# Kernel tuning notes

Hardware: AMD Instinct MI355X
Metric: run time of the kernel (lower is better)

The kernel has to match this reference:

```python
import jax, jax.numpy as jnp
import numpy as np
from jax import lax

TAU = 0.25
N_TIMESTEPS = 12
OUTPUT_TICKS = 4
INPUT_DIM = 1024
HIDDEN = 1024
OUTPUT_DIM = 1024
CLEANUP = 512
BATCH = 1024
W_SD = 0.1


def setup_inputs() -> dict:
    key = jax.random.key(0)
    ks = jax.random.split(key, 6)
    inputs = jax.random.normal(ks[0], (BATCH, N_TIMESTEPS, INPUT_DIM), dtype=jnp.float32)
    w_oh = W_SD * jax.random.normal(ks[1], (INPUT_DIM, HIDDEN), dtype=jnp.float32)
    w_hp = W_SD * jax.random.normal(ks[2], (HIDDEN, OUTPUT_DIM), dtype=jnp.float32)
    w_pp = W_SD * jax.random.normal(ks[3], (OUTPUT_DIM, OUTPUT_DIM), dtype=jnp.float32)
    w_pc = W_SD * jax.random.normal(ks[4], (OUTPUT_DIM, CLEANUP), dtype=jnp.float32)
    w_cp = W_SD * jax.random.normal(ks[5], (CLEANUP, OUTPUT_DIM), dtype=jnp.float32)
    bias_h = jnp.zeros((HIDDEN,), jnp.float32)
    bias_p = jnp.zeros((OUTPUT_DIM,), jnp.float32)
    bias_c = jnp.zeros((CLEANUP,), jnp.float32)
    return {"inputs": inputs, "w_oh": w_oh, "w_hp": w_hp, "w_pp": w_pp,
            "w_pc": w_pc, "w_cp": w_cp, "bias_h": bias_h, "bias_p": bias_p,
            "bias_c": bias_c}


def reference(inputs, w_oh, w_hp, w_pp, w_pc, w_cp, bias_h, bias_p, bias_c):
    B = inputs.shape[0]
    act = jax.nn.sigmoid
    # time-major input stream: step t consumes o_input[:, t-1, :]
    x = jnp.swapaxes(inputs, 0, 1)  # [T, B, I]

    in_h0 = jnp.zeros((B, HIDDEN), jnp.float32)
    in_p0 = jnp.zeros((B, OUTPUT_DIM), jnp.float32)
    in_c0 = jnp.zeros((B, CLEANUP), jnp.float32)
    carry0 = (in_h0, in_p0, in_c0, in_h0 + 0.5, in_p0 + 0.5, in_c0 + 0.5)

    def step(carry, o_t):
        in_h, in_p, in_c, a_h, a_p, a_c = carry
        # leaky-integrator blends; hp/pp/cp/pc all use PREVIOUS step activations
        h = TAU * (o_t @ w_oh + bias_h) + (1.0 - TAU) * in_h
        p = TAU * (a_h @ w_hp + a_p @ w_pp + a_c @ w_cp + bias_p) + (1.0 - TAU) * in_p
        c = TAU * (a_p @ w_pc + bias_c) + (1.0 - TAU) * in_c
        a_p_new = act(p)
        new_carry = (h, p, c, act(h), a_p_new, act(c))
        return new_carry, a_p_new

    _, act_p_seq = lax.scan(step, carry0, x)  # [T, B, OUTPUT_DIM]
    return act_p_seq[-OUTPUT_TICKS:]  # [OUTPUT_TICKS, B, OUTPUT_DIM]
```

## Files before the change

### kernel.cpp

```cpp
#include <hip/hip_runtime.h>
#include <cstdint>
#include <cstddef>


typedef _Float16 half8 __attribute__((ext_vector_type(8)));
typedef float floatx4 __attribute__((ext_vector_type(4)));

__device__ __forceinline__ void async_cp16(const void* g, void* l) {
  __builtin_amdgcn_global_load_lds(
      (const __attribute__((address_space(1))) void*)g,
      (__attribute__((address_space(3))) void*)l, 16, 0, 0);
}

__device__ __forceinline__ float sigmoidf_(float x) {
  return 1.f / (1.f + __expf(-x));
}

__global__ __launch_bounds__(256) void k_trans_all(
    const float* __restrict__ w_oh, const float* __restrict__ w_hp,
    _Float16* __restrict__ WohT, _Float16* __restrict__ Whp) {
  const float* src = blockIdx.z ? w_hp : w_oh;
  _Float16* dst = blockIdx.z ? Whp : WohT;
  __shared__ float tile[64][65];
  const int k0 = blockIdx.y * 64, n0 = blockIdx.x * 64;
  const int tx = threadIdx.x & 63, ty = threadIdx.x >> 6;
#pragma unroll
  for (int j = 0; j < 16; ++j) {
    int kr = j * 4 + ty;
    tile[kr][tx] = src[(size_t)(k0 + kr) * 1024 + n0 + tx];
  }
  __syncthreads();
#pragma unroll
  for (int j = 0; j < 16; ++j) {
    int nr = j * 4 + ty;
    dst[(size_t)(n0 + nr) * 1024 + k0 + tx] = (_Float16)tile[tx][nr];
  }
}

__global__ __launch_bounds__(256) void k_pack_all(
    const float* __restrict__ w_pp, const float* __restrict__ w_cp,
    const float* __restrict__ w_pc, _Float16* __restrict__ Wrf,
    _Float16* __restrict__ Wcf) {
  const int z = blockIdx.z;
  const float* src;
  _Float16* dst;
  int N, kStride, kOff;
  if (z == 0) {
    src = w_pp; dst = Wrf; N = 1024; kStride = 48; kOff = 0;
  } else if (z == 1) {
    if (blockIdx.y >= 8) return;
    src = w_cp; dst = Wrf; N = 1024; kStride = 48; kOff = 32;
  } else {
    if (blockIdx.x >= 8) return;
    src = w_pc; dst = Wcf; N = 512; kStride = 32; kOff = 0;
  }
  __shared__ float tile[64][65];
  const int k0 = blockIdx.y * 64, n0 = blockIdx.x * 64;
  const int tx = threadIdx.x & 63, ty = threadIdx.x >> 6;
#pragma unroll
  for (int jj = 0; jj < 16; ++jj) {
    int kr = jj * 4 + ty;
    tile[kr][tx] = src[(size_t)(k0 + kr) * N + n0 + tx];
  }
  __syncthreads();
  const int j = threadIdx.x >> 6, lane = threadIdx.x & 63;
  const int r16 = lane & 15, quad = lane >> 4;
#pragma unroll
  for (int c = 0; c < 2; ++c) {
    half8 v;
#pragma unroll
    for (int u = 0; u < 8; ++u)
      v[u] = (_Float16)tile[c * 32 + quad * 8 + u][j * 16 + r16];
    const int kcG = kOff + blockIdx.y * 2 + c;
    *(half8*)(dst + ((size_t)(blockIdx.x * kStride + kcG) * 4 + j) * 512 +
              lane * 8) = v;
  }
}

__global__ __launch_bounds__(256) void k_q0(
    const float* __restrict__ w_hp, const float* __restrict__ bias_p,
    _Float16* __restrict__ Q) {
  const int n = blockIdx.x * 256 + threadIdx.x;
  float s = 0.f;
  for (int k = 0; k < 1024; ++k) s += w_hp[(size_t)k * 1024 + n];
  const _Float16 q = (_Float16)(0.25f * (0.5f * s + bias_p[n]));
  for (int b = 0; b < 1024; ++b) Q[(size_t)b * 1024 + n] = q;
}

__global__ __launch_bounds__(256) void k_prep(
    const float* __restrict__ x, _Float16* __restrict__ U,
    _Float16* __restrict__ AP0, _Float16* __restrict__ AC0,
    float* __restrict__ Pst, float* __restrict__ Cst) {
  const int id = blockIdx.x * 256 + threadIdx.x;
  const int b = id >> 10, i = id & 1023;
  const float* xb = x + (size_t)b * 12 * 1024 + i;
  float g = 0.f;
#pragma unroll
  for (int t = 0; t < 11; ++t) {
    g = xb[t * 1024] + 0.75f * g;
    U[(size_t)t * 1048576 + id] = (_Float16)g;
  }
  AP0[id] = (_Float16)0.5f;
  Pst[id] = 0.f;
  if (i < 512) {
    const int cid = b * 512 + i;
    AC0[cid] = (_Float16)0.5f;
    Cst[cid] = 0.f;
  }
}

__global__ __launch_bounds__(256) void k_gemm_big(
    const _Float16* __restrict__ A, const _Float16* __restrict__ B,
    const float* __restrict__ bias, _Float16* __restrict__ dst, int mode) {
  __shared__ __align__(16) _Float16 sA[8192];
  __shared__ __align__(16) _Float16 sB[8192];
  const int lane = threadIdx.x & 63, w = threadIdx.x >> 6;
  const int mBase = blockIdx.y * 128, nBase = blockIdx.x * 128;
  const int r16 = lane & 15, quad = lane >> 4, mrow = lane >> 3;
  const int gsw = ((lane & 7) ^ (mrow & 7)) * 8;
  const floatx4 zero = {0.f, 0.f, 0.f, 0.f};
  floatx4 acc[4][4];
#pragma unroll
  for (int i = 0; i < 4; ++i)
#pragma unroll
    for (int j = 0; j < 4; ++j) acc[i][j] = zero;

  const _Float16* gbase =
      (w < 2 ? A + (size_t)(mBase + (w & 1) * 64 + mrow) * 1024
             : B + (size_t)(nBase + (w & 1) * 64 + mrow) * 1024) +
      gsw;
  _Float16* lbase = (w < 2 ? sA : sB) + (w & 1) * 4096;
  const int wi = w >> 1, wj = w & 1;
  const _Float16* csa = sA + wi * 4096;
  const _Float16* csb = sB + wj * 4096;

  for (int kt = 0; kt < 16; ++kt) {
    const int k0 = kt << 6;
#pragma unroll
    for (int q = 0; q < 8; ++q)
      async_cp16(gbase + (size_t)q * 8192 + k0, lbase + q * 512);
    asm volatile("s_waitcnt vmcnt(0)" ::: "memory");
    __syncthreads();
#pragma unroll
    for (int kk = 0; kk < 2; ++kk) {
      const int sw = ((kk * 4 + quad) ^ (r16 & 7)) * 8;
      half8 af[4], bf[4];
#pragma unroll
      for (int i = 0; i < 4; ++i) af[i] = *(const half8*)&csa[(i * 16 + r16) * 64 + sw];
#pragma unroll
      for (int j = 0; j < 4; ++j) bf[j] = *(const half8*)&csb[(j * 16 + r16) * 64 + sw];
#pragma unroll
      for (int i = 0; i < 4; ++i)
#pragma unroll
        for (int j = 0; j < 4; ++j)
          acc[i][j] =
              __builtin_amdgcn_mfma_f32_16x16x32_f16(af[i], bf[j], acc[i][j], 0, 0, 0);
    }
    __syncthreads();
  }

  const int rowQ = mBase + wi * 64;
  const int colQ = nBase + wj * 64;
  if (mode == 0) {
    const int tm1 = mBase >> 10;
    const float beta = 1.f - __powf(0.75f, (float)(tm1 + 1));
    _Float16* o = dst + (size_t)(rowQ + 1024) * 1024;
#pragma unroll
    for (int i = 0; i < 4; ++i)
#pragma unroll
      for (int j = 0; j < 4; ++j) {
        const int n = colQ + j * 16 + r16;
#pragma unroll
        for (int r = 0; r < 4; ++r) {
          const int row = i * 16 + quad * 4 + r;
          const float h = 0.25f * acc[i][j][r] + beta * bias[n];
          o[(size_t)row * 1024 + n] = (_Float16)sigmoidf_(h);
        }
      }
  } else {
    _Float16* o = dst + (size_t)rowQ * 1024;
#pragma unroll
    for (int i = 0; i < 4; ++i)
#pragma unroll
      for (int j = 0; j < 4; ++j) {
        const int n = colQ + j * 16 + r16;
#pragma unroll
        for (int r = 0; r < 4; ++r) {
          const int row = i * 16 + quad * 4 + r;
          o[(size_t)row * 1024 + n] = (_Float16)(0.25f * (acc[i][j][r] + bias[n]));
        }
      }
  }
}

__global__ __launch_bounds__(256, 3) void k_step(
    const _Float16* __restrict__ Qt, const _Float16* __restrict__ APc,
    const _Float16* __restrict__ ACc, _Float16* __restrict__ APn,
    _Float16* __restrict__ ACn, const _Float16* __restrict__ Wrf,
    const _Float16* __restrict__ Wcf, const float* __restrict__ bias_c,
    float* __restrict__ Pst, float* __restrict__ Cst,
    float* __restrict__ out_t) {
  __shared__ float red[4][2][4][4][64];
  const int lane = threadIdx.x & 63, w = threadIdx.x >> 6;
  const int r16 = lane & 15, quad = lane >> 4;
  const int blk = blockIdx.x;
  const bool isP = blk < 512;
  int mBase, nt;
  if (isP) {
    nt = (blk & 7) | ((blk & 256) ? 8 : 0);
    mBase = ((blk >> 3) & 31) * 32;
  } else {
    const int b = blk - 512;
    nt = b & 7;
    mBase = (b >> 3) * 32;
  }
  const int nBase = nt * 64;
  const floatx4 zero = {0.f, 0.f, 0.f, 0.f};
  floatx4 acc[2][4];
#pragma unroll
  for (int i = 0; i < 2; ++i)
#pragma unroll
    for (int j = 0; j < 4; ++j) acc[i][j] = zero;

  half8 abuf[4][2], bbuf[4][4];
  auto MM = [&](half8* af, half8* bf) {
#pragma unroll
    for (int i = 0; i < 2; ++i)
#pragma unroll
      for (int j = 0; j < 4; ++j)
        acc[i][j] = __builtin_amdgcn_mfma_f32_16x16x32_f16(af[i], bf[j],
                                                           acc[i][j], 0, 0, 0);
  };

  if (isP) {
    const int kcBase = w * 12;
    auto LD = [&](half8* af, half8* bf, int c) {
      const int kc = kcBase + c;
      const int kg = kc * 32;
      if (kc < 32) {
#pragma unroll
        for (int i = 0; i < 2; ++i)
          af[i] = *(const half8*)(APc + (size_t)(mBase + i * 16 + r16) * 1024 +
                                  kg + quad * 8);
      } else {
#pragma unroll
        for (int i = 0; i < 2; ++i)
          af[i] = *(const half8*)(ACc + (size_t)(mBase + i * 16 + r16) * 512 +
                                  (kg - 1024) + quad * 8);
      }
      const _Float16* wp = Wrf + (size_t)(nt * 48 + kc) * 2048 + lane * 8;
#pragma unroll
      for (int j = 0; j < 4; ++j) bf[j] = *(const half8*)(wp + j * 512);
    };
    LD(abuf[0], bbuf[0], 0);
    LD(abuf[1], bbuf[1], 1);
    LD(abuf[2], bbuf[2], 2);
#pragma unroll
    for (int c = 0; c < 12; ++c) {
      if (c + 3 < 12) LD(abuf[(c + 3) & 3], bbuf[(c + 3) & 3], c + 3);
      MM(abuf[c & 3], bbuf[c & 3]);
    }
  } else {
    const int kcBase = w * 8;
    auto LD = [&](half8* af, half8* bf, int c) {
      const int kc = kcBase + c;
      const int kg = kc * 32;
#pragma unroll
      for (int i = 0; i < 2; ++i)
        af[i] = *(const half8*)(APc + (size_t)(mBase + i * 16 + r16) * 1024 +
                                kg + quad * 8);
      const _Float16* wp = Wcf + (size_t)(nt * 32 + kc) * 2048 + lane * 8;
#pragma unroll
      for (int j = 0; j < 4; ++j) bf[j] = *(const half8*)(wp + j * 512);
    };
    LD(abuf[0], bbuf[0], 0);
    LD(abuf[1], bbuf[1], 1);
    LD(abuf[2], bbuf[2], 2);
#pragma unroll
    for (int c = 0; c < 8; ++c) {
      if (c + 3 < 8) LD(abuf[(c + 3) & 3], bbuf[(c + 3) & 3], c + 3);
      MM(abuf[c & 3], bbuf[c & 3]);
    }
  }

#pragma unroll
  for (int i = 0; i < 2; ++i)
#pragma unroll
    for (int j = 0; j < 4; ++j)
#pragma unroll
      for (int r = 0; r < 4; ++r) red[w][i][j][r][lane] = acc[i][j][r];
  __syncthreads();

  if (isP) {
#pragma unroll
    for (int i = 0; i < 2; ++i) {
      const int n = nBase + w * 16 + r16;
#pragma unroll
      for (int r = 0; r < 4; ++r) {
        const float v = red[0][i][w][r][lane] + red[1][i][w][r][lane] +
                        red[2][i][w][r][lane] + red[3][i][w][r][lane];
        const int b = mBase + i * 16 + quad * 4 + r;
        const size_t o = (size_t)b * 1024 + n;
        const float pn = 0.25f * v + (float)Qt[o] + 0.75f * Pst[o];
        Pst[o] = pn;
        const float a = sigmoidf_(pn);
        APn[o] = (_Float16)a;
        if (out_t) out_t[o] = a;
      }
    }
  } else {
#pragma unroll
    for (int i = 0; i < 2; ++i) {
      const int n = nBase + w * 16 + r16;
#pragma unroll
      for (int r = 0; r < 4; ++r) {
        const float v = red[0][i][w][r][lane] + red[1][i][w][r][lane] +
                        red[2][i][w][r][lane] + red[3][i][w][r][lane];
        const int b = mBase + i * 16 + quad * 4 + r;
        const size_t o = (size_t)b * 512 + n;
        const float cn = 0.25f * (v + bias_c[n]) + 0.75f * Cst[o];
        Cst[o] = cn;
        ACn[o] = (_Float16)sigmoidf_(cn);
      }
    }
  }
}

extern "C" void kernel_launch(void* const* d_in, const int* in_sizes, int n_in,
                              void* d_out, int out_size, void* d_ws,
                              size_t ws_size, hipStream_t stream) {
  const float* x      = (const float*)d_in[0];
  const float* w_oh   = (const float*)d_in[1];
  const float* w_hp   = (const float*)d_in[2];
  const float* w_pp   = (const float*)d_in[3];
  const float* w_pc   = (const float*)d_in[4];
  const float* w_cp   = (const float*)d_in[5];
  const float* bias_h = (const float*)d_in[6];
  const float* bias_p = (const float*)d_in[7];
  const float* bias_c = (const float*)d_in[8];
  float* out = (float*)d_out;

  uint8_t* p = (uint8_t*)d_ws;
  _Float16* Wrf  = (_Float16*)p; p += (size_t)1024 * 1536 * 2;
  _Float16* Wcf  = (_Float16*)p; p += (size_t)512 * 1024 * 2;
  _Float16* WohT = (_Float16*)p; p += (size_t)1024 * 1024 * 2;
  _Float16* Whp  = (_Float16*)p; p += (size_t)1024 * 1024 * 2;
  _Float16* U    = (_Float16*)p; p += (size_t)11 * 1048576 * 2;
  _Float16* AH   = (_Float16*)p; p += (size_t)12 * 1048576 * 2;
  _Float16* Q    = (_Float16*)p; p += (size_t)12 * 1048576 * 2;
  _Float16* AP0  = (_Float16*)p; p += (size_t)1048576 * 2;
  _Float16* AP1  = (_Float16*)p; p += (size_t)1048576 * 2;
  _Float16* AC0  = (_Float16*)p; p += (size_t)512 * 1024 * 2;
  _Float16* AC1  = (_Float16*)p; p += (size_t)512 * 1024 * 2;
  float* Pst = (float*)p; p += (size_t)1048576 * 4;
  float* Cst = (float*)p; p += (size_t)512 * 1024 * 4;

  const dim3 blk256(256);
  k_trans_all<<<dim3(16, 16, 2), blk256, 0, stream>>>(w_oh, w_hp, WohT, Whp);
  k_pack_all<<<dim3(16, 16, 3), blk256, 0, stream>>>(w_pp, w_cp, w_pc, Wrf, Wcf);
  k_q0<<<dim3(4), blk256, 0, stream>>>(w_hp, bias_p, Q);
  k_prep<<<4096, blk256, 0, stream>>>(x, U, AP0, AC0, Pst, Cst);
  k_gemm_big<<<dim3(8, 88), blk256, 0, stream>>>(U, WohT, bias_h, AH, 0);
  k_gemm_big<<<dim3(8, 88), blk256, 0, stream>>>(AH + 1048576, Whp, bias_p,
                                                 Q + 1048576, 1);
  for (int t = 0; t < 12; ++t) {
    const _Float16* APc = (t & 1) ? AP1 : AP0;
    _Float16* APn       = (t & 1) ? AP0 : AP1;
    const _Float16* ACc = (t & 1) ? AC1 : AC0;
    _Float16* ACn       = (t & 1) ? AC0 : AC1;
    float* ot = (t >= 8) ? out + (size_t)(t - 8) * 1048576 : (float*)nullptr;
    k_step<<<dim3(768), blk256, 0, stream>>>(Q + (size_t)t * 1048576, APc,
                                             ACc, APn, ACn, Wrf, Wcf, bias_c,
                                             Pst, Cst, ot);
  }
}
```

Baseline: 465.8 us.

## Replace LDS-tiled big GEMMs with register-direct fragment-packed GEMM and reshuffle step tiles

Drops the separate transpose kernel and packs w_oh and w_hp into the MFMA fragment layout inside the existing pack kernel. The two large precompute GEMMs now load A and pre-packed B fragments straight from global memory into registers with a 3-deep software pipeline, with no LDS staging or barriers, on 32x64 tiles per wave. The recurrent step kernel changes its block-to-tile mapping and prefetch depth from 3 to 2 buffers to cut register pressure. This removes the sync and LDS traffic but loses cross-wave reuse of B in LDS, so global and L2 traffic rises.

```diff
diff --git a/kernel.cpp b/kernel.cpp
--- a/kernel.cpp
+++ b/kernel.cpp
@@ -6,53 +6,28 @@
 typedef _Float16 half8 __attribute__((ext_vector_type(8)));
 typedef float floatx4 __attribute__((ext_vector_type(4)));
 
-__device__ __forceinline__ void async_cp16(const void* g, void* l) {
-  __builtin_amdgcn_global_load_lds(
-      (const __attribute__((address_space(1))) void*)g,
-      (__attribute__((address_space(3))) void*)l, 16, 0, 0);
-}
-
 __device__ __forceinline__ float sigmoidf_(float x) {
   return 1.f / (1.f + __expf(-x));
 }
 
-__global__ __launch_bounds__(256) void k_trans_all(
-    const float* __restrict__ w_oh, const float* __restrict__ w_hp,
-    _Float16* __restrict__ WohT, _Float16* __restrict__ Whp) {
-  const float* src = blockIdx.z ? w_hp : w_oh;
-  _Float16* dst = blockIdx.z ? Whp : WohT;
-  __shared__ float tile[64][65];
-  const int k0 = blockIdx.y * 64, n0 = blockIdx.x * 64;
-  const int tx = threadIdx.x & 63, ty = threadIdx.x >> 6;
-#pragma unroll
-  for (int j = 0; j < 16; ++j) {
-    int kr = j * 4 + ty;
-    tile[kr][tx] = src[(size_t)(k0 + kr) * 1024 + n0 + tx];
-  }
-  __syncthreads();
-#pragma unroll
-  for (int j = 0; j < 16; ++j) {
-    int nr = j * 4 + ty;
-    dst[(size_t)(n0 + nr) * 1024 + k0 + tx] = (_Float16)tile[tx][nr];
-  }
-}
-
 __global__ __launch_bounds__(256) void k_pack_all(
     const float* __restrict__ w_pp, const float* __restrict__ w_cp,
-    const float* __restrict__ w_pc, _Float16* __restrict__ Wrf,
-    _Float16* __restrict__ Wcf) {
+    const float* __restrict__ w_pc, const float* __restrict__ w_oh,
+    const float* __restrict__ w_hp, _Float16* __restrict__ Wrf,
+    _Float16* __restrict__ Wcf, _Float16* __restrict__ Wohf,
+    _Float16* __restrict__ Whpf) {
   const int z = blockIdx.z;
   const float* src;
   _Float16* dst;
   int N, kStride, kOff;
-  if (z == 0) {
-    src = w_pp; dst = Wrf; N = 1024; kStride = 48; kOff = 0;
-  } else if (z == 1) {
-    if (blockIdx.y >= 8) return;
-    src = w_cp; dst = Wrf; N = 1024; kStride = 48; kOff = 32;
-  } else {
-    if (blockIdx.x >= 8) return;
-    src = w_pc; dst = Wcf; N = 512; kStride = 32; kOff = 0;
+  switch (z) {
+    case 0: src = w_pp; dst = Wrf;  N = 1024; kStride = 48; kOff = 0;  break;
+    case 1: if (blockIdx.y >= 8) return;
+            src = w_cp; dst = Wrf;  N = 1024; kStride = 48; kOff = 32; break;
+    case 2: if (blockIdx.x >= 8) return;
+            src = w_pc; dst = Wcf;  N = 512;  kStride = 32; kOff = 0;  break;
+    case 3: src = w_oh; dst = Wohf; N = 1024; kStride = 32; kOff = 0;  break;
+    default:src = w_hp; dst = Whpf; N = 1024; kStride = 32; kOff = 0;  break;
   }
   __shared__ float tile[64][65];
   const int k0 = blockIdx.y * 64, n0 = blockIdx.x * 64;
@@ -109,67 +84,59 @@
   }
 }
 
-__global__ __launch_bounds__(256) void k_gemm_big(
-    const _Float16* __restrict__ A, const _Float16* __restrict__ B,
+__global__ __launch_bounds__(256, 3) void k_gemm_fp(
+    const _Float16* __restrict__ A, const _Float16* __restrict__ Bf,
     const float* __restrict__ bias, _Float16* __restrict__ dst, int mode) {
-  __shared__ __align__(16) _Float16 sA[8192];
-  __shared__ __align__(16) _Float16 sB[8192];
   const int lane = threadIdx.x & 63, w = threadIdx.x >> 6;
-  const int mBase = blockIdx.y * 128, nBase = blockIdx.x * 128;
-  const int r16 = lane & 15, quad = lane >> 4, mrow = lane >> 3;
-  const int gsw = ((lane & 7) ^ (mrow & 7)) * 8;
+  const int r16 = lane & 15, quad = lane >> 4;
+  const int mBase = (blockIdx.y * 4 + w) * 32;
+  const int nt = blockIdx.x;
   const floatx4 zero = {0.f, 0.f, 0.f, 0.f};
-  floatx4 acc[4][4];
-#pragma unroll
-  for (int i = 0; i < 4; ++i)
+  floatx4 acc[2][4];
+#pragma unroll
+  for (int i = 0; i < 2; ++i)
 #pragma unroll
     for (int j = 0; j < 4; ++j) acc[i][j] = zero;
 
-  const _Float16* gbase =
-      (w < 2 ? A + (size_t)(mBase + (w & 1) * 64 + mrow) * 1024
-             : B + (size_t)(nBase + (w & 1) * 64 + mrow) * 1024) +
-      gsw;
-  _Float16* lbase = (w < 2 ? sA : sB) + (w & 1) * 4096;
-  const int wi = w >> 1, wj = w & 1;
-  const _Float16* csa = sA + wi * 4096;
-  const _Float16* csb = sB + wj * 4096;
-
-  for (int kt = 0; kt < 16; ++kt) {
-    const int k0 = kt << 6;
-#pragma unroll
-    for (int q = 0; q < 8; ++q)
-      async_cp16(gbase + (size_t)q * 8192 + k0, lbase + q * 512);
-    asm volatile("s_waitcnt vmcnt(0)" ::: "memory");
-    __syncthreads();
-#pragma unroll
-    for (int kk = 0; kk < 2; ++kk) {
-      const int sw = ((kk * 4 + quad) ^ (r16 & 7)) * 8;
-      half8 af[4], bf[4];
-#pragma unroll
-      for (int i = 0; i < 4; ++i) af[i] = *(const half8*)&csa[(i * 16 + r16) * 64 + sw];
-#pragma unroll
-      for (int j = 0; j < 4; ++j) bf[j] = *(const half8*)&csb[(j * 16 + r16) * 64 + sw];
-#pragma unroll
-      for (int i = 0; i < 4; ++i)
-#pragma unroll
-        for (int j = 0; j < 4; ++j)
-          acc[i][j] =
-              __builtin_amdgcn_mfma_f32_16x16x32_f16(af[i], bf[j], acc[i][j], 0, 0, 0);
-    }
-    __syncthreads();
-  }
-
-  const int rowQ = mBase + wi * 64;
-  const int colQ = nBase + wj * 64;
+  const _Float16* A0 = A + (size_t)(mBase + r16) * 1024 + quad * 8;
+  const _Float16* A1 = A0 + 16 * 1024;
+  const _Float16* wb = Bf + (size_t)nt * 32 * 2048 + lane * 8;
+
+  half8 ab[3][2], bb[3][4];
+  auto LD = [&](int c, int buf) {
+    const int kg = c * 32;
+    ab[buf][0] = *(const half8*)(A0 + kg);
+    ab[buf][1] = *(const half8*)(A1 + kg);
+    const _Float16* wp = wb + (size_t)c * 2048;
+#pragma unroll
+    for (int j = 0; j < 4; ++j) bb[buf][j] = *(const half8*)(wp + j * 512);
+  };
+  auto MM = [&](int buf) {
+#pragma unroll
+    for (int i = 0; i < 2; ++i)
+#pragma unroll
+      for (int j = 0; j < 4; ++j)
+        acc[i][j] = __builtin_amdgcn_mfma_f32_16x16x32_f16(
+            ab[buf][i], bb[buf][j], acc[i][j], 0, 0, 0);
+  };
+
+  LD(0, 0);
+  LD(1, 1);
+#pragma unroll
+  for (int c = 0; c < 32; ++c) {
+    if (c + 2 < 32) LD(c + 2, (c + 2) % 3);
+    MM(c % 3);
+  }
+
   if (mode == 0) {
-    const int tm1 = mBase >> 10;
-    const float beta = 1.f - __powf(0.75f, (float)(tm1 + 1));
-    _Float16* o = dst + (size_t)(rowQ + 1024) * 1024;
-#pragma unroll
-    for (int i = 0; i < 4; ++i)
+    const int t = (mBase >> 10) + 1;
+    const float beta = 1.f - __powf(0.75f, (float)t);
+    _Float16* o = dst + (size_t)(mBase + 1024) * 1024;
+#pragma unroll
+    for (int i = 0; i < 2; ++i)
 #pragma unroll
       for (int j = 0; j < 4; ++j) {
-        const int n = colQ + j * 16 + r16;
+        const int n = nt * 64 + j * 16 + r16;
 #pragma unroll
         for (int r = 0; r < 4; ++r) {
           const int row = i * 16 + quad * 4 + r;
@@ -178,12 +145,12 @@
         }
       }
   } else {
-    _Float16* o = dst + (size_t)rowQ * 1024;
-#pragma unroll
-    for (int i = 0; i < 4; ++i)
+    _Float16* o = dst + (size_t)mBase * 1024;
+#pragma unroll
+    for (int i = 0; i < 2; ++i)
 #pragma unroll
       for (int j = 0; j < 4; ++j) {
-        const int n = colQ + j * 16 + r16;
+        const int n = nt * 64 + j * 16 + r16;
 #pragma unroll
         for (int r = 0; r < 4; ++r) {
           const int row = i * 16 + quad * 4 + r;
@@ -207,12 +174,12 @@
   const bool isP = blk < 512;
   int mBase, nt;
   if (isP) {
-    nt = (blk & 7) | ((blk & 256) ? 8 : 0);
-    mBase = ((blk >> 3) & 31) * 32;
+    mBase = (blk >> 4) * 32;
+    nt = blk & 15;
   } else {
     const int b = blk - 512;
+    mBase = (b >> 3) * 32;
     nt = b & 7;
-    mBase = (b >> 3) * 32;
   }
   const int nBase = nt * 64;
   const floatx4 zero = {0.f, 0.f, 0.f, 0.f};
@@ -222,7 +189,7 @@
 #pragma unroll
     for (int j = 0; j < 4; ++j) acc[i][j] = zero;
 
-  half8 abuf[4][2], bbuf[4][4];
+  half8 abuf[3][2], bbuf[3][4];
   auto MM = [&](half8* af, half8* bf) {
 #pragma unroll
     for (int i = 0; i < 2; ++i)
@@ -254,11 +221,10 @@
     };
     LD(abuf[0], bbuf[0], 0);
     LD(abuf[1], bbuf[1], 1);
-    LD(abuf[2], bbuf[2], 2);
 #pragma unroll
     for (int c = 0; c < 12; ++c) {
-      if (c + 3 < 12) LD(abuf[(c + 3) & 3], bbuf[(c + 3) & 3], c + 3);
-      MM(abuf[c & 3], bbuf[c & 3]);
+      if (c + 2 < 12) LD(abuf[(c + 2) % 3], bbuf[(c + 2) % 3], c + 2);
+      MM(abuf[c % 3], bbuf[c % 3]);
     }
   } else {
     const int kcBase = w * 8;
@@ -275,11 +241,10 @@
     };
     LD(abuf[0], bbuf[0], 0);
     LD(abuf[1], bbuf[1], 1);
-    LD(abuf[2], bbuf[2], 2);
 #pragma unroll
     for (int c = 0; c < 8; ++c) {
-      if (c + 3 < 8) LD(abuf[(c + 3) & 3], bbuf[(c + 3) & 3], c + 3);
-      MM(abuf[c & 3], bbuf[c & 3]);
+      if (c + 2 < 8) LD(abuf[(c + 2) % 3], bbuf[(c + 2) % 3], c + 2);
+      MM(abuf[c % 3], bbuf[c % 3]);
     }
   }
 
@@ -343,8 +308,8 @@
   uint8_t* p = (uint8_t*)d_ws;
   _Float16* Wrf  = (_Float16*)p; p += (size_t)1024 * 1536 * 2;
   _Float16* Wcf  = (_Float16*)p; p += (size_t)512 * 1024 * 2;
-  _Float16* WohT = (_Float16*)p; p += (size_t)1024 * 1024 * 2;
-  _Float16* Whp  = (_Float16*)p; p += (size_t)1024 * 1024 * 2;
+  _Float16* Wohf = (_Float16*)p; p += (size_t)1024 * 1024 * 2;
+  _Float16* Whpf = (_Float16*)p; p += (size_t)1024 * 1024 * 2;
   _Float16* U    = (_Float16*)p; p += (size_t)11 * 1048576 * 2;
   _Float16* AH   = (_Float16*)p; p += (size_t)12 * 1048576 * 2;
   _Float16* Q    = (_Float16*)p; p += (size_t)12 * 1048576 * 2;
@@ -356,12 +321,12 @@
   float* Cst = (float*)p; p += (size_t)512 * 1024 * 4;
 
   const dim3 blk256(256);
-  k_trans_all<<<dim3(16, 16, 2), blk256, 0, stream>>>(w_oh, w_hp, WohT, Whp);
-  k_pack_all<<<dim3(16, 16, 3), blk256, 0, stream>>>(w_pp, w_cp, w_pc, Wrf, Wcf);
+  k_pack_all<<<dim3(16, 16, 5), blk256, 0, stream>>>(w_pp, w_cp, w_pc, w_oh,
+                                                     w_hp, Wrf, Wcf, Wohf, Whpf);
   k_q0<<<dim3(4), blk256, 0, stream>>>(w_hp, bias_p, Q);
   k_prep<<<4096, blk256, 0, stream>>>(x, U, AP0, AC0, Pst, Cst);
-  k_gemm_big<<<dim3(8, 88), blk256, 0, stream>>>(U, WohT, bias_h, AH, 0);
-  k_gemm_big<<<dim3(8, 88), blk256, 0, stream>>>(AH + 1048576, Whp, bias_p,
+  k_gemm_fp<<<dim3(16, 88), blk256, 0, stream>>>(U, Wohf, bias_h, AH, 0);
+  k_gemm_fp<<<dim3(16, 88), blk256, 0, stream>>>(AH + 1048576, Whpf, bias_p,
                                                  Q + 1048576, 1);
   for (int t = 0; t < 12; ++t) {
     const _Float16* APc = (t & 1) ? AP1 : AP0;
```

Result: slower. 511.3 us (+9.8%).
